# Optimization experiments

Measured on AMD Instinct MI355X. Metric: run time of the kernel, lower is better.

Reference implementation:

```python
import jax, jax.numpy as jnp
import numpy as np

PHI = 1.6
JITTER = 1e-4
ETA = 1.0
BETA = 0.5
EPS_CHOL = 1e-6
R_NEIGH = 2


def _solve3(L, d):
    # lower-triangular 3x3 forward substitution; L broadcasts against d[..., 3]
    y0 = d[..., 0] / L[..., 0, 0]
    y1 = (d[..., 1] - L[..., 1, 0] * y0) / L[..., 1, 1]
    y2 = (d[..., 2] - L[..., 2, 0] * y0 - L[..., 2, 1] * y1) / L[..., 2, 2]
    return jnp.stack([y0, y1, y2], axis=-1)


def _overlap_score(delta, L):
    # fused_gaussian_overlap_score: Gaussian log-overlap ~ -0.5*(Mahalanobis + logdet)
    y = _solve3(L, delta)
    maha = jnp.sum(y * y, axis=-1)
    logdet = 2.0 * jnp.sum(jnp.log(jnp.diagonal(L, axis1=-2, axis2=-1)), axis=-1)
    return -0.5 * (maha + logdet)


def _head(x, ln_g, ln_b, W1, b1, W2, b2):
    # LayerNorm -> Linear -> SiLU -> Linear(->1), squeeze
    m = jnp.mean(x, axis=-1, keepdims=True)
    v = jnp.var(x, axis=-1, keepdims=True)
    h = (x - m) / jnp.sqrt(v + 1e-5) * ln_g + ln_b
    h = jax.nn.silu(h @ W1 + b1)
    return (h @ W2 + b2)[..., 0]


def setup_inputs() -> dict:
    key = jax.random.key(0)
    ks = jax.random.split(key, 12)
    B, Kp, M, C = 2, 1024, 8, 256
    s_parent = jax.random.normal(ks[0], (B, Kp, C), jnp.float32)
    mu_p = jax.random.normal(ks[1], (B, Kp, 3), jnp.float32) * 10.0
    A = jax.random.normal(ks[2], (B, Kp, 3, 3), jnp.float32) * 0.5
    Sigma_p = jnp.einsum('bkij,bklj->bkil', A, A) + 0.05 * jnp.eye(3, dtype=jnp.float32)
    mask_parent = jnp.ones((B, Kp), jnp.float32)
    xi_noise = jax.random.normal(ks[3], (B, Kp, M, 3), jnp.float32)
    emb = jax.random.normal(ks[4], (M, C), jnp.float32) * 0.02
    lin = lambda k, fi, fo, s=0.02: jax.random.normal(k, (fi, fo), jnp.float32) * s
    return dict(
        s_parent=s_parent, mu_p=mu_p, Sigma_p=Sigma_p, mask_parent=mask_parent,
        xi_noise=xi_noise, emb=emb,
        gate_ln_g=jnp.ones((C,), jnp.float32), gate_ln_b=jnp.zeros((C,), jnp.float32),
        gate_W1=lin(ks[5], C, C), gate_b1=jnp.zeros((C,), jnp.float32),
        gate_W2=lin(ks[6], C, 1), gate_b2=jnp.zeros((1,), jnp.float32),
        prior_ln_g=jnp.ones((C,), jnp.float32), prior_ln_b=jnp.zeros((C,), jnp.float32),
        prior_W1=lin(ks[7], C, C), prior_b1=jnp.zeros((C,), jnp.float32),
        prior_W2=lin(ks[8], C, 1), prior_b2=jnp.zeros((1,), jnp.float32),
        geom_W=lin(ks[9], C, 3, 0.01), geom_b=jnp.zeros((3,), jnp.float32),
        K_target=6144,
    )


def reference(s_parent, mu_p, Sigma_p, mask_parent, xi_noise, emb,
              gate_ln_g, gate_ln_b, gate_W1, gate_b1, gate_W2, gate_b2,
              prior_ln_g, prior_ln_b, prior_W1, prior_b1, prior_W2, prior_b2,
              geom_W, geom_b, K_target):
    B, Kp, C = s_parent.shape
    M = emb.shape[0]
    Kc = Kp * M
    I3 = jnp.eye(3, dtype=s_parent.dtype)

    # --- candidate children from per-parent Cholesky splat ---
    Lp = jnp.linalg.cholesky(Sigma_p + EPS_CHOL * I3)               # [B,Kp,3,3]
    xi = xi_noise + (emb @ geom_W + geom_b)                          # [B,Kp,M,3]
    mu0 = mu_p[:, :, None, :] + jnp.einsum('bkae,bkme->bkma', Lp, xi)
    mu0 = mu0.reshape(B, Kc, 3)

    j0 = jnp.repeat(jnp.arange(Kp), M)                               # [Kc] birth parent
    t_ids = jnp.tile(jnp.arange(M), Kp)                              # [Kc] child slot
    m0 = mask_parent[:, j0]

    # --- gate g ---
    gate_in = s_parent[:, j0, :] + emb[t_ids]                        # [B,Kc,C]
    b = _head(gate_in, gate_ln_g, gate_ln_b, gate_W1, gate_b1, gate_W2, gate_b2)
    a = jax.nn.softplus(_head(s_parent, prior_ln_g, prior_ln_b, prior_W1, prior_b1, prior_W2, prior_b2))
    b = b + BETA * jnp.log(a[:, j0] + 1e-8)
    g = jax.nn.sigmoid(b / max(ETA, 1e-6)) * m0                      # [B,Kc]
    loss_count = jnp.mean((jnp.sum(g, axis=1) - float(K_target)) ** 2)

    # --- top-R neighbor parents by overlap score (indices only, no grad) ---
    mu0_birth = mu_p[:, j0, :]                                       # mu of birth parent
    delta1 = mu0_birth[:, :, None, :] - mu_p[:, None, :, :]          # [B,Kc,Kp,3]
    score1 = _overlap_score(delta1, Lp[:, None])                     # [B,Kc,Kp]
    self_hot = (jnp.arange(Kp)[None, :] == j0[:, None])              # [Kc,Kp]
    score1 = jnp.where(self_hot[None], 1e9, score1)
    _, neigh = jax.lax.top_k(jax.lax.stop_gradient(score1), R_NEIGH) # [B,Kc,R], col0=j0

    bidx = jnp.arange(B)[:, None, None]
    mu_nei = mu_p[bidx, neigh]                                       # [B,Kc,R,3]
    Sig_nei = Sigma_p[bidx, neigh]                                   # [B,Kc,R,3,3]
    L_nei = Lp[bidx, neigh]
    s_nei = s_parent[bidx, neigh]                                    # [B,Kc,R,C]

    # --- soft responsibilities over the R neighbors ---
    score2 = _overlap_score(mu0[:, :, None, :] - mu_nei, L_nei)      # [B,Kc,R]
    w = jax.nn.softmax(score2, axis=-1)

    # --- moment-matching refine (sparse form of B_resp: rows of B are w scattered at neigh) ---
    mu_child = jnp.einsum('bir,bird->bid', w, mu_nei)                # [B,Kc,3]
    intra = jnp.einsum('bir,birmn->bimn', w, Sig_nei) * PHI ** (-2)
    dmu = mu_nei - mu_child[:, :, None, :]
    inter = jnp.einsum('bir,birm,birn->bimn', w, dmu, dmu)
    Sigma_child = intra + inter + JITTER * I3                        # [B,Kc,3,3]

    s_mix = jnp.einsum('bir,birc->bic', w, s_nei)
    s_child0 = g[..., None] * s_mix                                  # [B,Kc,C]
    return s_child0, mu_child, Sigma_child, g, loss_count
```

## Files before the change

kernel.cpp:

```cpp
#include <hip/hip_runtime.h>
#include <math.h>

#define NPAR 2048
#define KP   1024
#define MM   8
#define CC   256
#define KC   8192
#define NCH  16384

#define WS_PAR    0
#define WS_MEANSP 26624
#define WS_SUMSQ  28672
#define WS_DOT8   30720
#define WS_APRIOR 47104
#define WS_EGATE  49152
#define WS_UGATE  51200
#define WS_C0GATE 51456
#define WS_GEO    51712
#define WS_MEANE  51736
#define WS_SUMSQE 51744
#define WS_NEIGH  51752
#define WS_PGATE  53824

#define OUT_S    0
#define OUT_MU   4194304
#define OUT_SIG  4243456
#define OUT_G    4390912
#define OUT_LOSS 4407296

__device__ __forceinline__ float siluf(float x){ return x / (1.f + expf(-x)); }
__device__ __forceinline__ float softplusf(float x){ return x > 20.f ? x : log1pf(expf(x)); }

__global__ __launch_bounds__(256) void kA(const float* __restrict__ sp,
                                          const float* __restrict__ mu_p,
                                          const float* __restrict__ Sig,
                                          const float* __restrict__ emb,
                                          const float* __restrict__ geom_W,
                                          const float* __restrict__ geom_b,
                                          float* __restrict__ ws) {
  int blk = blockIdx.x;
  int t = threadIdx.x;
  if (blk < 512) {
    int pid  = blk * 4 + (t >> 6);
    int lane = t & 63;
    const float4 v = *(const float4*)(sp + pid * CC + lane * 4);
    float s  = v.x + v.y + v.z + v.w;
    float ss = v.x*v.x + v.y*v.y + v.z*v.z + v.w*v.w;
    float pd[8];
#pragma unroll
    for (int m = 0; m < 8; m++) {
      float4 e = *(const float4*)(emb + m * CC + lane * 4);
      pd[m] = v.x*e.x + v.y*e.y + v.z*e.z + v.w*e.w;
    }
#pragma unroll
    for (int o = 32; o > 0; o >>= 1) {
      s  += __shfl_xor(s, o);
      ss += __shfl_xor(ss, o);
#pragma unroll
      for (int m = 0; m < 8; m++) pd[m] += __shfl_xor(pd[m], o);
    }
    if (lane == 0) {
      ws[WS_MEANSP + pid] = s * (1.f / 256.f);
      ws[WS_SUMSQ + pid]  = ss;
#pragma unroll
      for (int m = 0; m < 8; m++) ws[WS_DOT8 + pid * 8 + m] = pd[m];
    }
  } else if (blk < 520) {
    int pid = (blk - 512) * 256 + t;
    const float* S = Sig + pid * 9;
    float a00 = S[0] + 1e-6f, a10 = S[3], a11 = S[4] + 1e-6f;
    float a20 = S[6], a21 = S[7], a22 = S[8] + 1e-6f;
    float L00 = sqrtf(a00); float i0 = 1.f / L00;
    float L10 = a10 * i0, L20 = a20 * i0;
    float L11 = sqrtf(a11 - L10 * L10); float i1 = 1.f / L11;
    float L21 = (a21 - L20 * L10) * i1;
    float L22 = sqrtf(a22 - L20 * L20 - L21 * L21); float i2 = 1.f / L22;
    float logdet = 2.f * (logf(L00) + logf(L11) + logf(L22));
    float* P = ws + WS_PAR;
    P[0*NPAR+pid]=L00; P[1*NPAR+pid]=L10; P[2*NPAR+pid]=L11;
    P[3*NPAR+pid]=L20; P[4*NPAR+pid]=L21; P[5*NPAR+pid]=L22;
    P[6*NPAR+pid]=i0;  P[7*NPAR+pid]=i1;  P[8*NPAR+pid]=i2;
    P[9*NPAR+pid]=logdet;
    P[10*NPAR+pid]=mu_p[pid*3+0]; P[11*NPAR+pid]=mu_p[pid*3+1]; P[12*NPAR+pid]=mu_p[pid*3+2];
  } else {
    if (t < 192) {
      int o = t >> 3, lane8 = t & 7;
      int m = o / 3, d = o % 3;
      float acc = 0.f;
      for (int k = lane8; k < 256; k += 8) acc += emb[m * 256 + k] * geom_W[k * 3 + d];
      acc += __shfl_xor(acc, 1); acc += __shfl_xor(acc, 2); acc += __shfl_xor(acc, 4);
      if (lane8 == 0) ws[WS_GEO + o] = acc + geom_b[d];
    } else {
      int o = (t - 192) >> 3, lane8 = t & 7;
      if (o < 8) {
        float s = 0.f, ss = 0.f;
        for (int k = lane8; k < 256; k += 8) { float e = emb[o * 256 + k]; s += e; ss += e * e; }
        s  += __shfl_xor(s, 1);  s  += __shfl_xor(s, 2);  s  += __shfl_xor(s, 4);
        ss += __shfl_xor(ss, 1); ss += __shfl_xor(ss, 2); ss += __shfl_xor(ss, 4);
        if (lane8 == 0) { ws[WS_MEANE + o] = s * (1.f / 256.f); ws[WS_SUMSQE + o] = ss; }
      }
    }
  }
}

__global__ __launch_bounds__(256) void kE(float* __restrict__ ws) {
  int wv = blockIdx.x * 4 + (threadIdx.x >> 6);
  int lane = threadIdx.x & 63;
  int b = wv >> 10;
  int j = wv & (KP - 1);
  const float* P = ws + WS_PAR;
  float qx = P[10*NPAR+wv], qy = P[11*NPAR+wv], qz = P[12*NPAR+wv];
  float best = -3.4e38f; int bidx = 1 << 30;
  for (int it = 0; it < 16; it++) {
    int k = it * 64 + lane;
    int idx = b * KP + k;
    float L10 = P[1*NPAR+idx], L20 = P[3*NPAR+idx], L21 = P[4*NPAR+idx];
    float i0 = P[6*NPAR+idx], i1 = P[7*NPAR+idx], i2 = P[8*NPAR+idx];
    float ld = P[9*NPAR+idx];
    float dx = qx - P[10*NPAR+idx], dy = qy - P[11*NPAR+idx], dz = qz - P[12*NPAR+idx];
    float y0 = dx * i0;
    float y1 = (dy - L10 * y0) * i1;
    float y2 = (dz - L20 * y0 - L21 * y1) * i2;
    float sc = -0.5f * (y0*y0 + y1*y1 + y2*y2 + ld);
    if (k == j) sc = -3.4e38f;
    if (sc > best || (sc == best && k < bidx)) { best = sc; bidx = k; }
  }
#pragma unroll
  for (int o = 32; o > 0; o >>= 1) {
    float ob = __shfl_xor(best, o);
    int   oi = __shfl_xor(bidx, o);
    if (ob > best || (ob == best && oi < bidx)) { best = ob; bidx = oi; }
  }
  if (lane == 0) ((int*)ws)[WS_NEIGH + wv] = bidx;
}

__global__ __launch_bounds__(256) void kC(const float* __restrict__ sp,
                                          const float* __restrict__ emb,
                                          const float* __restrict__ g_ln_g,
                                          const float* __restrict__ g_ln_b,
                                          const float* __restrict__ gW1,
                                          const float* __restrict__ gb1,
                                          const float* __restrict__ p_ln_g,
                                          const float* __restrict__ p_ln_b,
                                          const float* __restrict__ pW1,
                                          const float* __restrict__ pb1,
                                          const float* __restrict__ pW2,
                                          const float* __restrict__ pb2,
                                          float* __restrict__ ws) {
  __shared__ float xs[8][256];
  __shared__ float red[4][8];
  int blk = blockIdx.x;
  int t = threadIdx.x;
  bool prior = (blk >= 256 && blk < 512);
  const float* W1 = prior ? pW1 : gW1;

  if (blk < 256) {
    int base = blk * 8;
    float g = g_ln_g[t];
#pragma unroll
    for (int r = 0; r < 8; r++) xs[r][t] = sp[(base + r) * 256 + t] * g;
  } else if (blk < 512) {
    int base = (blk - 256) * 8;
    float pg = p_ln_g[t], pbv = p_ln_b[t];
#pragma unroll
    for (int r = 0; r < 8; r++) {
      int row = base + r;
      float mean = ws[WS_MEANSP + row];
      float var  = ws[WS_SUMSQ + row] * (1.f / 256.f) - mean * mean;
      float rstd = rsqrtf(var + 1e-5f);
      xs[r][t] = (sp[row * 256 + t] - mean) * rstd * pg + pbv;
    }
  } else if (blk == 512) {
    float g = g_ln_g[t];
#pragma unroll
    for (int r = 0; r < 8; r++) xs[r][t] = emb[r * 256 + t] * g;
  } else {
    xs[0][t] = g_ln_g[t];
    xs[1][t] = g_ln_b[t];
#pragma unroll
    for (int r = 2; r < 8; r++) xs[r][t] = 0.f;
  }
  __syncthreads();

  float acc[8] = {0,0,0,0,0,0,0,0};
  for (int k = 0; k < 256; k++) {
    float w = W1[k * 256 + t];
#pragma unroll
    for (int r = 0; r < 8; r++) acc[r] += xs[r][k] * w;
  }

  if (blk < 256) {
    int base = blk * 8;
#pragma unroll
    for (int r = 0; r < 8; r++) ws[WS_PGATE + (base + r) * 256 + t] = acc[r];
  } else if (blk < 512) {
    int base = (blk - 256) * 8;
    float b1 = pb1[t], w2 = pW2[t];
    float tv[8];
#pragma unroll
    for (int r = 0; r < 8; r++) {
      float h = acc[r] + b1;
      tv[r] = siluf(h) * w2;
    }
#pragma unroll
    for (int o = 32; o > 0; o >>= 1) {
#pragma unroll
      for (int r = 0; r < 8; r++) tv[r] += __shfl_xor(tv[r], o);
    }
    int wave = t >> 6;
    if ((t & 63) == 0) {
#pragma unroll
      for (int r = 0; r < 8; r++) red[wave][r] = tv[r];
    }
    __syncthreads();
    if (t < 8) {
      float sum = red[0][t] + red[1][t] + red[2][t] + red[3][t] + pb2[0];
      ws[WS_APRIOR + base + t] = softplusf(sum);
    }
  } else if (blk == 512) {
#pragma unroll
    for (int r = 0; r < 8; r++) ws[WS_EGATE + r * 256 + t] = acc[r];
  } else {
    ws[WS_UGATE + t]  = acc[0];
    ws[WS_C0GATE + t] = acc[1] + gb1[t];
  }
}

__global__ __launch_bounds__(256) void kD(const float* __restrict__ sp,
                                          const float* __restrict__ Sig,
                                          const float* __restrict__ mask,
                                          const float* __restrict__ xi_noise,
                                          const float* __restrict__ gW2,
                                          const float* __restrict__ gb2,
                                          const float* __restrict__ ws,
                                          float* __restrict__ out) {
  int wv   = blockIdx.x * 4 + (threadIdx.x >> 6);
  int lane = threadIdx.x & 63;
  int b = wv >> 13;
  int i = wv & (KC - 1);
  int j = i >> 3;
  int m = i & 7;
  int prow = b * KP + j;

  float mean_x = ws[WS_MEANSP + prow] + ws[WS_MEANE + m];
  float Ex2 = ws[WS_SUMSQ + prow] + 2.f * ws[WS_DOT8 + prow * 8 + m] + ws[WS_SUMSQE + m];
  float var = Ex2 * (1.f / 256.f) - mean_x * mean_x;
  float rstd = rsqrtf(var + 1e-5f);

  int c4 = lane * 4;
  float Pv[4], Ev[4], Uv[4], C0v[4], W2v[4];
  *(float4*)Pv  = *(const float4*)(ws + WS_PGATE + prow * 256 + c4);
  *(float4*)Ev  = *(const float4*)(ws + WS_EGATE + m * 256 + c4);
  *(float4*)Uv  = *(const float4*)(ws + WS_UGATE + c4);
  *(float4*)C0v = *(const float4*)(ws + WS_C0GATE + c4);
  *(float4*)W2v = *(const float4*)(gW2 + c4);
  float partial = 0.f;
#pragma unroll
  for (int q = 0; q < 4; q++) {
    float pre = (Pv[q] + Ev[q] - mean_x * Uv[q]) * rstd + C0v[q];
    partial += siluf(pre) * W2v[q];
  }
#pragma unroll
  for (int o = 32; o > 0; o >>= 1) partial += __shfl_xor(partial, o);
  float aP = ws[WS_APRIOR + prow];
  float bval = partial + gb2[0] + 0.5f * logf(aP + 1e-8f);
  float g = (1.f / (1.f + expf(-bval))) * mask[prow];

  const float* PP = ws + WS_PAR;
  float L00 = PP[0*NPAR+prow], L10 = PP[1*NPAR+prow], L11 = PP[2*NPAR+prow];
  float L20 = PP[3*NPAR+prow], L21 = PP[4*NPAR+prow], L22 = PP[5*NPAR+prow];
  float mx = PP[10*NPAR+prow], my = PP[11*NPAR+prow], mz = PP[12*NPAR+prow];
  int xbase = (prow * 8 + m) * 3;
  float x0 = xi_noise[xbase + 0] + ws[WS_GEO + m * 3 + 0];
  float x1 = xi_noise[xbase + 1] + ws[WS_GEO + m * 3 + 1];
  float x2 = xi_noise[xbase + 2] + ws[WS_GEO + m * 3 + 2];
  float m0x = mx + L00 * x0;
  float m0y = my + L10 * x0 + L11 * x1;
  float m0z = mz + L20 * x0 + L21 * x1 + L22 * x2;

  int n1 = ((const int*)ws)[WS_NEIGH + prow];
  int nrow[2]; nrow[0] = prow; nrow[1] = b * KP + n1;
  float sc[2], nx[2], ny[2], nz[2];
#pragma unroll
  for (int r = 0; r < 2; r++) {
    int q = nrow[r];
    float i0 = PP[6*NPAR+q], i1 = PP[7*NPAR+q], i2 = PP[8*NPAR+q], ld = PP[9*NPAR+q];
    float l10 = PP[1*NPAR+q], l20 = PP[3*NPAR+q], l21 = PP[4*NPAR+q];
    nx[r] = PP[10*NPAR+q]; ny[r] = PP[11*NPAR+q]; nz[r] = PP[12*NPAR+q];
    float dx = m0x - nx[r], dy = m0y - ny[r], dz = m0z - nz[r];
    float y0 = dx * i0;
    float y1 = (dy - l10 * y0) * i1;
    float y2 = (dz - l20 * y0 - l21 * y1) * i2;
    sc[r] = -0.5f * (y0*y0 + y1*y1 + y2*y2 + ld);
  }
  float mxs = fmaxf(sc[0], sc[1]);
  float e0 = expf(sc[0] - mxs), e1 = expf(sc[1] - mxs);
  float inv = 1.f / (e0 + e1);
  float w0 = e0 * inv, w1 = e1 * inv;

  float mcx = w0 * nx[0] + w1 * nx[1];
  float mcy = w0 * ny[0] + w1 * ny[1];
  float mcz = w0 * nz[0] + w1 * nz[1];

  float d0x = nx[0] - mcx, d0y = ny[0] - mcy, d0z = nz[0] - mcz;
  float d1x = nx[1] - mcx, d1y = ny[1] - mcy, d1z = nz[1] - mcz;
  const float* S0 = Sig + nrow[0] * 9;
  const float* S1 = Sig + nrow[1] * 9;
  const float PHIm2 = 0.390625f;
  float Sout[9];
  float dd0[3] = {d0x, d0y, d0z};
  float dd1[3] = {d1x, d1y, d1z};
#pragma unroll
  for (int a = 0; a < 3; a++)
#pragma unroll
    for (int e = 0; e < 3; e++) {
      float v = (w0 * S0[a*3+e] + w1 * S1[a*3+e]) * PHIm2
              + w0 * dd0[a] * dd0[e] + w1 * dd1[a] * dd1[e];
      if (a == e) v += 1e-4f;
      Sout[a*3+e] = v;
    }

  if (lane == 0) {
    float* om = out + OUT_MU + wv * 3;
    om[0] = mcx; om[1] = mcy; om[2] = mcz;
    out[OUT_G + wv] = g;
    float* os = out + OUT_SIG + wv * 9;
#pragma unroll
    for (int q = 0; q < 9; q++) os[q] = Sout[q];
  }

  float s0v[4], s1v[4], ov[4];
  *(float4*)s0v = *(const float4*)(sp + nrow[0] * 256 + c4);
  *(float4*)s1v = *(const float4*)(sp + nrow[1] * 256 + c4);
  float gw0 = g * w0, gw1 = g * w1;
#pragma unroll
  for (int q = 0; q < 4; q++) ov[q] = gw0 * s0v[q] + gw1 * s1v[q];
  *(float4*)(out + OUT_S + wv * 256 + c4) = *(float4*)ov;
}

__global__ __launch_bounds__(256) void kF(const float* __restrict__ out_in,
                                          const int* __restrict__ Kt,
                                          float* __restrict__ out) {
  __shared__ float red[4][2];
  int t = threadIdx.x;
  const float* gp = out_in + OUT_G;
  float s0 = 0.f, s1 = 0.f;
  for (int it = 0; it < 32; it++) {
    s0 += gp[it * 256 + t];
    s1 += gp[KC + it * 256 + t];
  }
#pragma unroll
  for (int o = 32; o > 0; o >>= 1) {
    s0 += __shfl_xor(s0, o);
    s1 += __shfl_xor(s1, o);
  }
  int wave = t >> 6;
  if ((t & 63) == 0) { red[wave][0] = s0; red[wave][1] = s1; }
  __syncthreads();
  if (t == 0) {
    float S0 = red[0][0] + red[1][0] + red[2][0] + red[3][0];
    float S1 = red[0][1] + red[1][1] + red[2][1] + red[3][1];
    float K = (float)Kt[0];
    float l0 = S0 - K, l1 = S1 - K;
    out[OUT_LOSS] = 0.5f * (l0 * l0 + l1 * l1);
  }
}

extern "C" void kernel_launch(void* const* d_in, const int* in_sizes, int n_in,
                              void* d_out, int out_size, void* d_ws, size_t ws_size,
                              hipStream_t stream) {
  const float* s_parent   = (const float*)d_in[0];
  const float* mu_p       = (const float*)d_in[1];
  const float* Sigma_p    = (const float*)d_in[2];
  const float* mask_par   = (const float*)d_in[3];
  const float* xi_noise   = (const float*)d_in[4];
  const float* emb        = (const float*)d_in[5];
  const float* gate_ln_g  = (const float*)d_in[6];
  const float* gate_ln_b  = (const float*)d_in[7];
  const float* gate_W1    = (const float*)d_in[8];
  const float* gate_b1    = (const float*)d_in[9];
  const float* gate_W2    = (const float*)d_in[10];
  const float* gate_b2    = (const float*)d_in[11];
  const float* prior_ln_g = (const float*)d_in[12];
  const float* prior_ln_b = (const float*)d_in[13];
  const float* prior_W1   = (const float*)d_in[14];
  const float* prior_b1   = (const float*)d_in[15];
  const float* prior_W2   = (const float*)d_in[16];
  const float* prior_b2   = (const float*)d_in[17];
  const float* geom_W     = (const float*)d_in[18];
  const float* geom_b     = (const float*)d_in[19];
  const int*   K_target   = (const int*)d_in[20];

  float* ws  = (float*)d_ws;
  float* out = (float*)d_out;

  kA<<<521, 256, 0, stream>>>(s_parent, mu_p, Sigma_p, emb, geom_W, geom_b, ws);
  kE<<<NPAR / 4, 256, 0, stream>>>(ws);
  kC<<<514, 256, 0, stream>>>(s_parent, emb, gate_ln_g, gate_ln_b, gate_W1, gate_b1,
                              prior_ln_g, prior_ln_b, prior_W1, prior_b1, prior_W2, prior_b2, ws);
  kD<<<NCH / 4, 256, 0, stream>>>(s_parent, Sigma_p, mask_par, xi_noise, gate_W2, gate_b2,
                                  ws, out);
  kF<<<1, 256, 0, stream>>>(out, K_target, out);
}
```

Baseline: 161.3 us.

## Merge prep kernels into one launch and fold loss reduction into kD

Folds the three preparation kernels (parent stats/Cholesky, nearest-neighbor search, MLP heads) into a single launch. The neighbor search recomputes the Cholesky factors directly from Sigma, and the prior LayerNorm computes its own row statistics, which removes the dependencies between the former kernels. The final loss kernel is replaced by per-block atomic accumulation of gate sums in kD, with a ticket counter so the last block writes the loss. This cuts five launches to two and their serialization gaps, at the cost of redundant Cholesky work in the neighbor search and atomic contention on two addresses.

```diff
diff --git a/kernel.cpp b/kernel.cpp
--- a/kernel.cpp
+++ b/kernel.cpp
@@ -20,6 +20,8 @@
 #define WS_MEANE  51736
 #define WS_SUMSQE 51744
 #define WS_NEIGH  51752
+#define WS_GSUM   53800
+#define WS_TICKET 53802
 #define WS_PGATE  53824
 
 #define OUT_S    0
@@ -31,15 +33,31 @@
 __device__ __forceinline__ float siluf(float x){ return x / (1.f + expf(-x)); }
 __device__ __forceinline__ float softplusf(float x){ return x > 20.f ? x : log1pf(expf(x)); }
 
-__global__ __launch_bounds__(256) void kA(const float* __restrict__ sp,
+__global__ __launch_bounds__(256) void kP(const float* __restrict__ sp,
                                           const float* __restrict__ mu_p,
                                           const float* __restrict__ Sig,
                                           const float* __restrict__ emb,
                                           const float* __restrict__ geom_W,
                                           const float* __restrict__ geom_b,
+                                          const float* __restrict__ g_ln_g,
+                                          const float* __restrict__ g_ln_b,
+                                          const float* __restrict__ gW1,
+                                          const float* __restrict__ gb1,
+                                          const float* __restrict__ p_ln_g,
+                                          const float* __restrict__ p_ln_b,
+                                          const float* __restrict__ pW1,
+                                          const float* __restrict__ pb1,
+                                          const float* __restrict__ pW2,
+                                          const float* __restrict__ pb2,
                                           float* __restrict__ ws) {
+  __shared__ float xs[8][256];
+  __shared__ float red[4][8];
+  __shared__ float redS[4][8];
+  __shared__ float redQ[4][8];
+  __shared__ float mv[2][8];
   int blk = blockIdx.x;
   int t = threadIdx.x;
+
   if (blk < 512) {
     int pid  = blk * 4 + (t >> 6);
     int lane = t & 63;
@@ -75,14 +93,18 @@
     float L11 = sqrtf(a11 - L10 * L10); float i1 = 1.f / L11;
     float L21 = (a21 - L20 * L10) * i1;
     float L22 = sqrtf(a22 - L20 * L20 - L21 * L21); float i2 = 1.f / L22;
-    float logdet = 2.f * (logf(L00) + logf(L11) + logf(L22));
+    float logdet = 2.f * logf(L00 * L11 * L22);
     float* P = ws + WS_PAR;
     P[0*NPAR+pid]=L00; P[1*NPAR+pid]=L10; P[2*NPAR+pid]=L11;
     P[3*NPAR+pid]=L20; P[4*NPAR+pid]=L21; P[5*NPAR+pid]=L22;
     P[6*NPAR+pid]=i0;  P[7*NPAR+pid]=i1;  P[8*NPAR+pid]=i2;
     P[9*NPAR+pid]=logdet;
     P[10*NPAR+pid]=mu_p[pid*3+0]; P[11*NPAR+pid]=mu_p[pid*3+1]; P[12*NPAR+pid]=mu_p[pid*3+2];
-  } else {
+  } else if (blk == 520) {
+    if (t == 0) {
+      ws[WS_GSUM + 0] = 0.f; ws[WS_GSUM + 1] = 0.f;
+      ((unsigned*)ws)[WS_TICKET] = 0u;
+    }
     if (t < 192) {
       int o = t >> 3, lane8 = t & 7;
       int m = o / 3, d = o % 3;
@@ -100,129 +122,137 @@
         if (lane8 == 0) { ws[WS_MEANE + o] = s * (1.f / 256.f); ws[WS_SUMSQE + o] = ss; }
       }
     }
-  }
-}
-
-__global__ __launch_bounds__(256) void kE(float* __restrict__ ws) {
-  int wv = blockIdx.x * 4 + (threadIdx.x >> 6);
-  int lane = threadIdx.x & 63;
-  int b = wv >> 10;
-  int j = wv & (KP - 1);
-  const float* P = ws + WS_PAR;
-  float qx = P[10*NPAR+wv], qy = P[11*NPAR+wv], qz = P[12*NPAR+wv];
-  float best = -3.4e38f; int bidx = 1 << 30;
-  for (int it = 0; it < 16; it++) {
-    int k = it * 64 + lane;
-    int idx = b * KP + k;
-    float L10 = P[1*NPAR+idx], L20 = P[3*NPAR+idx], L21 = P[4*NPAR+idx];
-    float i0 = P[6*NPAR+idx], i1 = P[7*NPAR+idx], i2 = P[8*NPAR+idx];
-    float ld = P[9*NPAR+idx];
-    float dx = qx - P[10*NPAR+idx], dy = qy - P[11*NPAR+idx], dz = qz - P[12*NPAR+idx];
-    float y0 = dx * i0;
-    float y1 = (dy - L10 * y0) * i1;
-    float y2 = (dz - L20 * y0 - L21 * y1) * i2;
-    float sc = -0.5f * (y0*y0 + y1*y1 + y2*y2 + ld);
-    if (k == j) sc = -3.4e38f;
-    if (sc > best || (sc == best && k < bidx)) { best = sc; bidx = k; }
-  }
-#pragma unroll
-  for (int o = 32; o > 0; o >>= 1) {
-    float ob = __shfl_xor(best, o);
-    int   oi = __shfl_xor(bidx, o);
-    if (ob > best || (ob == best && oi < bidx)) { best = ob; bidx = oi; }
-  }
-  if (lane == 0) ((int*)ws)[WS_NEIGH + wv] = bidx;
-}
-
-__global__ __launch_bounds__(256) void kC(const float* __restrict__ sp,
-                                          const float* __restrict__ emb,
-                                          const float* __restrict__ g_ln_g,
-                                          const float* __restrict__ g_ln_b,
-                                          const float* __restrict__ gW1,
-                                          const float* __restrict__ gb1,
-                                          const float* __restrict__ p_ln_g,
-                                          const float* __restrict__ p_ln_b,
-                                          const float* __restrict__ pW1,
-                                          const float* __restrict__ pb1,
-                                          const float* __restrict__ pW2,
-                                          const float* __restrict__ pb2,
-                                          float* __restrict__ ws) {
-  __shared__ float xs[8][256];
-  __shared__ float red[4][8];
-  int blk = blockIdx.x;
-  int t = threadIdx.x;
-  bool prior = (blk >= 256 && blk < 512);
-  const float* W1 = prior ? pW1 : gW1;
-
-  if (blk < 256) {
-    int base = blk * 8;
-    float g = g_ln_g[t];
-#pragma unroll
-    for (int r = 0; r < 8; r++) xs[r][t] = sp[(base + r) * 256 + t] * g;
-  } else if (blk < 512) {
-    int base = (blk - 256) * 8;
-    float pg = p_ln_g[t], pbv = p_ln_b[t];
-#pragma unroll
-    for (int r = 0; r < 8; r++) {
-      int row = base + r;
-      float mean = ws[WS_MEANSP + row];
-      float var  = ws[WS_SUMSQ + row] * (1.f / 256.f) - mean * mean;
-      float rstd = rsqrtf(var + 1e-5f);
-      xs[r][t] = (sp[row * 256 + t] - mean) * rstd * pg + pbv;
-    }
-  } else if (blk == 512) {
-    float g = g_ln_g[t];
-#pragma unroll
-    for (int r = 0; r < 8; r++) xs[r][t] = emb[r * 256 + t] * g;
+  } else if (blk < 1033) {
+    int wv = (blk - 521) * 4 + (t >> 6);
+    int lane = t & 63;
+    int b = wv >> 10;
+    int j = wv & (KP - 1);
+    float qx = mu_p[wv*3+0], qy = mu_p[wv*3+1], qz = mu_p[wv*3+2];
+    float best = -3.4e38f; int bidx = 1 << 30;
+    for (int it = 0; it < 16; it++) {
+      int k = it * 64 + lane;
+      int idx = b * KP + k;
+      const float* S = Sig + idx * 9;
+      float a00 = S[0] + 1e-6f, a10 = S[3], a11 = S[4] + 1e-6f;
+      float a20 = S[6], a21 = S[7], a22 = S[8] + 1e-6f;
+      float L00 = sqrtf(a00); float i0 = 1.f / L00;
+      float L10 = a10 * i0, L20 = a20 * i0;
+      float L11 = sqrtf(a11 - L10 * L10); float i1 = 1.f / L11;
+      float L21 = (a21 - L20 * L10) * i1;
+      float L22 = sqrtf(a22 - L20 * L20 - L21 * L21); float i2 = 1.f / L22;
+      float ld = 2.f * logf(L00 * L11 * L22);
+      float dx = qx - mu_p[idx*3+0], dy = qy - mu_p[idx*3+1], dz = qz - mu_p[idx*3+2];
+      float y0 = dx * i0;
+      float y1 = (dy - L10 * y0) * i1;
+      float y2 = (dz - L20 * y0 - L21 * y1) * i2;
+      float sc = -0.5f * (y0*y0 + y1*y1 + y2*y2 + ld);
+      if (k == j) sc = -3.4e38f;
+      if (sc > best || (sc == best && k < bidx)) { best = sc; bidx = k; }
+    }
+#pragma unroll
+    for (int o = 32; o > 0; o >>= 1) {
+      float ob = __shfl_xor(best, o);
+      int   oi = __shfl_xor(bidx, o);
+      if (ob > best || (ob == best && oi < bidx)) { best = ob; bidx = oi; }
+    }
+    if (lane == 0) ((int*)ws)[WS_NEIGH + wv] = bidx;
   } else {
-    xs[0][t] = g_ln_g[t];
-    xs[1][t] = g_ln_b[t];
-#pragma unroll
-    for (int r = 2; r < 8; r++) xs[r][t] = 0.f;
-  }
-  __syncthreads();
-
-  float acc[8] = {0,0,0,0,0,0,0,0};
-  for (int k = 0; k < 256; k++) {
-    float w = W1[k * 256 + t];
-#pragma unroll
-    for (int r = 0; r < 8; r++) acc[r] += xs[r][k] * w;
-  }
-
-  if (blk < 256) {
-    int base = blk * 8;
-#pragma unroll
-    for (int r = 0; r < 8; r++) ws[WS_PGATE + (base + r) * 256 + t] = acc[r];
-  } else if (blk < 512) {
-    int base = (blk - 256) * 8;
-    float b1 = pb1[t], w2 = pW2[t];
-    float tv[8];
-#pragma unroll
-    for (int r = 0; r < 8; r++) {
-      float h = acc[r] + b1;
-      tv[r] = siluf(h) * w2;
-    }
-#pragma unroll
-    for (int o = 32; o > 0; o >>= 1) {
-#pragma unroll
-      for (int r = 0; r < 8; r++) tv[r] += __shfl_xor(tv[r], o);
-    }
-    int wave = t >> 6;
-    if ((t & 63) == 0) {
-#pragma unroll
-      for (int r = 0; r < 8; r++) red[wave][r] = tv[r];
+    int cblk = blk - 1033;
+    bool prior = (cblk >= 256 && cblk < 512);
+    const float* W1 = prior ? pW1 : gW1;
+
+    if (cblk < 256) {
+      int base = cblk * 8;
+      float g = g_ln_g[t];
+#pragma unroll
+      for (int r = 0; r < 8; r++) xs[r][t] = sp[(base + r) * 256 + t] * g;
+    } else if (cblk < 512) {
+      int base = (cblk - 256) * 8;
+      float vr[8], s1[8], s2[8];
+#pragma unroll
+      for (int r = 0; r < 8; r++) {
+        vr[r] = sp[(base + r) * 256 + t];
+        s1[r] = vr[r];
+        s2[r] = vr[r] * vr[r];
+      }
+#pragma unroll
+      for (int o = 32; o > 0; o >>= 1) {
+#pragma unroll
+        for (int r = 0; r < 8; r++) { s1[r] += __shfl_xor(s1[r], o); s2[r] += __shfl_xor(s2[r], o); }
+      }
+      int wave = t >> 6;
+      if ((t & 63) == 0) {
+#pragma unroll
+        for (int r = 0; r < 8; r++) { redS[wave][r] = s1[r]; redQ[wave][r] = s2[r]; }
+      }
+      __syncthreads();
+      if (t < 8) {
+        float sum = redS[0][t] + redS[1][t] + redS[2][t] + redS[3][t];
+        float sq  = redQ[0][t] + redQ[1][t] + redQ[2][t] + redQ[3][t];
+        float mean = sum * (1.f / 256.f);
+        float var  = sq * (1.f / 256.f) - mean * mean;
+        mv[0][t] = mean;
+        mv[1][t] = rsqrtf(var + 1e-5f);
+      }
+      __syncthreads();
+      float pg = p_ln_g[t], pbv = p_ln_b[t];
+#pragma unroll
+      for (int r = 0; r < 8; r++)
+        xs[r][t] = (vr[r] - mv[0][r]) * mv[1][r] * pg + pbv;
+    } else if (cblk == 512) {
+      float g = g_ln_g[t];
+#pragma unroll
+      for (int r = 0; r < 8; r++) xs[r][t] = emb[r * 256 + t] * g;
+    } else {
+      xs[0][t] = g_ln_g[t];
+      xs[1][t] = g_ln_b[t];
+#pragma unroll
+      for (int r = 2; r < 8; r++) xs[r][t] = 0.f;
     }
     __syncthreads();
-    if (t < 8) {
-      float sum = red[0][t] + red[1][t] + red[2][t] + red[3][t] + pb2[0];
-      ws[WS_APRIOR + base + t] = softplusf(sum);
-    }
-  } else if (blk == 512) {
-#pragma unroll
-    for (int r = 0; r < 8; r++) ws[WS_EGATE + r * 256 + t] = acc[r];
-  } else {
-    ws[WS_UGATE + t]  = acc[0];
-    ws[WS_C0GATE + t] = acc[1] + gb1[t];
+
+    float acc[8] = {0,0,0,0,0,0,0,0};
+    for (int k = 0; k < 256; k++) {
+      float w = W1[k * 256 + t];
+#pragma unroll
+      for (int r = 0; r < 8; r++) acc[r] += xs[r][k] * w;
+    }
+
+    if (cblk < 256) {
+      int base = cblk * 8;
+#pragma unroll
+      for (int r = 0; r < 8; r++) ws[WS_PGATE + (base + r) * 256 + t] = acc[r];
+    } else if (cblk < 512) {
+      int base = (cblk - 256) * 8;
+      float b1 = pb1[t], w2 = pW2[t];
+      float tv[8];
+#pragma unroll
+      for (int r = 0; r < 8; r++) {
+        float h = acc[r] + b1;
+        tv[r] = siluf(h) * w2;
+      }
+#pragma unroll
+      for (int o = 32; o > 0; o >>= 1) {
+#pragma unroll
+        for (int r = 0; r < 8; r++) tv[r] += __shfl_xor(tv[r], o);
+      }
+      int wave = t >> 6;
+      if ((t & 63) == 0) {
+#pragma unroll
+        for (int r = 0; r < 8; r++) red[wave][r] = tv[r];
+      }
+      __syncthreads();
+      if (t < 8) {
+        float sum = red[0][t] + red[1][t] + red[2][t] + red[3][t] + pb2[0];
+        ws[WS_APRIOR + base + t] = softplusf(sum);
+      }
+    } else if (cblk == 512) {
+#pragma unroll
+      for (int r = 0; r < 8; r++) ws[WS_EGATE + r * 256 + t] = acc[r];
+    } else {
+      ws[WS_UGATE + t]  = acc[0];
+      ws[WS_C0GATE + t] = acc[1] + gb1[t];
+    }
   }
 }
 
@@ -232,9 +262,12 @@
                                           const float* __restrict__ xi_noise,
                                           const float* __restrict__ gW2,
                                           const float* __restrict__ gb2,
-                                          const float* __restrict__ ws,
+                                          const int* __restrict__ Kt,
+                                          float* __restrict__ ws,
                                           float* __restrict__ out) {
-  int wv   = blockIdx.x * 4 + (threadIdx.x >> 6);
+  __shared__ float gred[4];
+  int wave = threadIdx.x >> 6;
+  int wv   = blockIdx.x * 4 + wave;
   int lane = threadIdx.x & 63;
   int b = wv >> 13;
   int i = wv & (KC - 1);
@@ -265,6 +298,7 @@
   float aP = ws[WS_APRIOR + prow];
   float bval = partial + gb2[0] + 0.5f * logf(aP + 1e-8f);
   float g = (1.f / (1.f + expf(-bval))) * mask[prow];
+  if (lane == 0) gred[wave] = g;
 
   const float* PP = ws + WS_PAR;
   float L00 = PP[0*NPAR+prow], L10 = PP[1*NPAR+prow], L11 = PP[2*NPAR+prow];
@@ -336,33 +370,21 @@
 #pragma unroll
   for (int q = 0; q < 4; q++) ov[q] = gw0 * s0v[q] + gw1 * s1v[q];
   *(float4*)(out + OUT_S + wv * 256 + c4) = *(float4*)ov;
-}
-
-__global__ __launch_bounds__(256) void kF(const float* __restrict__ out_in,
-                                          const int* __restrict__ Kt,
-                                          float* __restrict__ out) {
-  __shared__ float red[4][2];
-  int t = threadIdx.x;
-  const float* gp = out_in + OUT_G;
-  float s0 = 0.f, s1 = 0.f;
-  for (int it = 0; it < 32; it++) {
-    s0 += gp[it * 256 + t];
-    s1 += gp[KC + it * 256 + t];
-  }
-#pragma unroll
-  for (int o = 32; o > 0; o >>= 1) {
-    s0 += __shfl_xor(s0, o);
-    s1 += __shfl_xor(s1, o);
-  }
-  int wave = t >> 6;
-  if ((t & 63) == 0) { red[wave][0] = s0; red[wave][1] = s1; }
+
   __syncthreads();
-  if (t == 0) {
-    float S0 = red[0][0] + red[1][0] + red[2][0] + red[3][0];
-    float S1 = red[0][1] + red[1][1] + red[2][1] + red[3][1];
-    float K = (float)Kt[0];
-    float l0 = S0 - K, l1 = S1 - K;
-    out[OUT_LOSS] = 0.5f * (l0 * l0 + l1 * l1);
+  if (threadIdx.x == 0) {
+    float bs = gred[0] + gred[1] + gred[2] + gred[3];
+    atomicAdd(ws + WS_GSUM + b, bs);
+    __threadfence();
+    unsigned tk = atomicAdd((unsigned*)ws + WS_TICKET, 1u);
+    if (tk == (NCH / 4) - 1) {
+      __threadfence();
+      float S0r = atomicAdd(ws + WS_GSUM + 0, 0.f);
+      float S1r = atomicAdd(ws + WS_GSUM + 1, 0.f);
+      float K = (float)Kt[0];
+      float l0 = S0r - K, l1 = S1r - K;
+      out[OUT_LOSS] = 0.5f * (l0 * l0 + l1 * l1);
+    }
   }
 }
 
@@ -394,11 +416,10 @@
   float* ws  = (float*)d_ws;
   float* out = (float*)d_out;
 
-  kA<<<521, 256, 0, stream>>>(s_parent, mu_p, Sigma_p, emb, geom_W, geom_b, ws);
-  kE<<<NPAR / 4, 256, 0, stream>>>(ws);
-  kC<<<514, 256, 0, stream>>>(s_parent, emb, gate_ln_g, gate_ln_b, gate_W1, gate_b1,
-                              prior_ln_g, prior_ln_b, prior_W1, prior_b1, prior_W2, prior_b2, ws);
-  kD<<<NCH / 4, 256, 0, stream>>>(s_parent, Sigma_p, mask_par, xi_noise, gate_W2, gate_b2,
-                                  ws, out);
-  kF<<<1, 256, 0, stream>>>(out, K_target, out);
+  kP<<<1547, 256, 0, stream>>>(s_parent, mu_p, Sigma_p, emb, geom_W, geom_b,
+                               gate_ln_g, gate_ln_b, gate_W1, gate_b1,
+                               prior_ln_g, prior_ln_b, prior_W1, prior_b1,
+                               prior_W2, prior_b2, ws);
+  kD<<<NCH / 4, 256, 0, stream>>>(s_parent, Sigma_p, mask_par, xi_noise,
+                                  gate_W2, gate_b2, K_target, ws, out);
 }
```

New measurement: 264.2 us. +63.8%, slower.
